# Performance work log

Hardware: AMD Instinct MI355X
Metric: run time of the kernel (lower is better)

## Reference

```python
import jax, jax.numpy as jnp
import numpy as np


def setup_inputs() -> dict:
    key = jax.random.key(0)
    N, E, LENGTH, DIM = 50000, 800000, 128, 128
    k1, k2, k3 = jax.random.split(key, 3)
    x = jax.random.normal(k1, (N, LENGTH), dtype=jnp.float32)
    edge_index = jax.random.randint(k2, (2, E), 0, N, dtype=jnp.int32)
    W = jax.random.normal(k3, (LENGTH, DIM), dtype=jnp.float32) / np.sqrt(LENGTH).astype(np.float32)
    b = jnp.zeros((DIM,), dtype=jnp.float32)
    return {"x": x, "edge_index": edge_index, "W": W, "b": b, "length": LENGTH, "dim": DIM}


def reference(x, edge_index, W, b, length, dim):
    # GCNConv(length, dim) with default add_self_loops + symmetric normalization,
    # then ReLU and softmax over the feature axis (dim=1).
    N = x.shape[0]
    src, dst = edge_index[0], edge_index[1]  # messages flow src -> dst (PyG source_to_target)
    loop = jnp.arange(N, dtype=src.dtype)
    src = jnp.concatenate([src, loop])
    dst = jnp.concatenate([dst, loop])
    # degree (incl. self-loops) computed on destination nodes, as in PyG gcn_norm
    deg = jax.ops.segment_sum(jnp.ones(dst.shape, dtype=x.dtype), dst, num_segments=N)
    dinv = jnp.where(deg > 0, jax.lax.rsqrt(deg), 0.0)
    norm = dinv[src] * dinv[dst]  # [E+N]
    xw = x @ W  # [N, dim] -- transform before propagate (in >= out here)
    msgs = xw[src] * norm[:, None]  # [E+N, dim] gather + scale
    out = jax.ops.segment_sum(msgs, dst, num_segments=N) + b  # scatter-add
    out = jax.nn.relu(out)
    return jax.nn.softmax(out, axis=1)
```

## Files before the change

kernel.cpp:

```cpp
#include <hip/hip_runtime.h>
#include <hip/hip_bf16.h>


#define KDIM 128
#define CAP 48
#define BSTRIDE 5120
#define GPAD 32

typedef __attribute__((ext_vector_type(8))) short bf16x8;
typedef __attribute__((ext_vector_type(4))) float f32x4;

__device__ __forceinline__ unsigned short f2bf(float f) {
    union { float f; unsigned u; } v; v.f = f;
    unsigned r = v.u + 0x7fff + ((v.u >> 16) & 1);
    return (unsigned short)(r >> 16);
}
__device__ __forceinline__ float bflo(unsigned u) {
    union { unsigned u; float f; } v; v.u = u << 16; return v.f;
}
__device__ __forceinline__ float bfhi(unsigned u) {
    union { unsigned u; float f; } v; v.u = u & 0xffff0000u; return v.f;
}

#define WPAD 72

__global__ __launch_bounds__(256) void fused_k(const float* __restrict__ x,
                                               const float* __restrict__ W,
                                               const int* __restrict__ src,
                                               const int* __restrict__ dst,
                                               int* __restrict__ gcount,
                                               unsigned int* __restrict__ gbuck,
                                               unsigned short* __restrict__ xwh,
                                               int N, int E, int GB, int nbuck) {
    __shared__ unsigned short Wl[128 * WPAD];
    __shared__ int hist[256];
    __shared__ int gbase_s[256];

    const int tid = threadIdx.x;

    if ((int)blockIdx.x >= GB) {
        int base = ((int)blockIdx.x - GB) * 2048;
        hist[tid] = 0;
        __syncthreads();

        unsigned ev[8];
        int bn[8], lr[8];
#pragma unroll
        for (int j = 0; j < 8; ++j) {
            int e = base + j * 256 + tid;
            bn[j] = -1;
            if (e < E) {
                int d = dst[e];
                int s = src[e];
                ev[j] = ((unsigned)d << 16) | (unsigned)s;
                bn[j] = d >> 8;
                lr[j] = atomicAdd(&hist[bn[j]], 1);
            }
        }
        __syncthreads();

        if (tid < nbuck && hist[tid] > 0)
            gbase_s[tid] = atomicAdd(&gcount[tid * GPAD], hist[tid]);
        __syncthreads();

#pragma unroll
        for (int j = 0; j < 8; ++j) {
            if (bn[j] >= 0) {
                int slot = gbase_s[bn[j]] + lr[j];
                if (slot < BSTRIDE)
                    gbuck[(size_t)bn[j] * BSTRIDE + slot] = ev[j];
            }
        }
        return;
    }

    const int lane = tid & 63;
    const int wv = tid >> 6;
    const int m15 = lane & 15;
    const int quad = lane >> 4;
    const int rbase = (int)blockIdx.x * 128;

    f32x4 acc[2][8];
#pragma unroll
    for (int st = 0; st < 2; ++st)
#pragma unroll
        for (int nb = 0; nb < 8; ++nb) acc[st][nb] = (f32x4){0.f, 0.f, 0.f, 0.f};

    for (int kc = 0; kc < KDIM; kc += 64) {
#pragma unroll
        for (int i = 0; i < 8; ++i) {
            int p = tid + 256 * i;
            int kk = p >> 5;
            int c4 = p & 31;
            float4 v = *(const float4*)(&W[(size_t)(kc + kk) * KDIM + c4 * 4]);
            int n0 = c4 * 4;
            Wl[(n0 + 0) * WPAD + kk] = f2bf(v.x);
            Wl[(n0 + 1) * WPAD + kk] = f2bf(v.y);
            Wl[(n0 + 2) * WPAD + kk] = f2bf(v.z);
            Wl[(n0 + 3) * WPAD + kk] = f2bf(v.w);
        }
        __syncthreads();

#pragma unroll
        for (int s2 = 0; s2 < 2; ++s2) {
            int k0 = kc + s2 * 32 + quad * 8;
            bf16x8 afr[2];
#pragma unroll
            for (int st = 0; st < 2; ++st) {
                int gr = rbase + wv * 32 + st * 16 + m15;
                int cr = min(gr, N - 1);
                const float4* xp = (const float4*)(&x[(size_t)cr * KDIM + k0]);
                float4 xa = xp[0], xb = xp[1];
                bf16x8 f;
                f[0] = (short)f2bf(xa.x); f[1] = (short)f2bf(xa.y);
                f[2] = (short)f2bf(xa.z); f[3] = (short)f2bf(xa.w);
                f[4] = (short)f2bf(xb.x); f[5] = (short)f2bf(xb.y);
                f[6] = (short)f2bf(xb.z); f[7] = (short)f2bf(xb.w);
                afr[st] = f;
            }
            int kk0 = s2 * 32 + quad * 8;
#pragma unroll
            for (int nb = 0; nb < 8; ++nb) {
                bf16x8 bfr = *(const bf16x8*)(&Wl[(nb * 16 + m15) * WPAD + kk0]);
#pragma unroll
                for (int st = 0; st < 2; ++st)
                    acc[st][nb] = __builtin_amdgcn_mfma_f32_16x16x32_bf16(
                        afr[st], bfr, acc[st][nb], 0, 0, 0);
            }
        }
        __syncthreads();
    }

#pragma unroll
    for (int st = 0; st < 2; ++st) {
        int rowbase = rbase + wv * 32 + st * 16 + quad * 4;
#pragma unroll
        for (int r = 0; r < 4; ++r) {
            int gr = rowbase + r;
            if (gr < N) {
#pragma unroll
                for (int nb = 0; nb < 8; ++nb)
                    xwh[(size_t)gr * KDIM + nb * 16 + m15] = f2bf(acc[st][nb][r]);
            }
        }
    }
}

__global__ __launch_bounds__(256) void build_k(const unsigned int* __restrict__ gbuck,
                                               const int* __restrict__ gcount,
                                               int* __restrict__ degi,
                                               unsigned short* __restrict__ csr,
                                               int N) {
    __shared__ unsigned int eb[BSTRIDE];
    __shared__ unsigned short cl[256 * CAP];
    __shared__ int cnts[256];

    const int tid = threadIdx.x;
    const int b = (int)blockIdx.x;
    const int cnt = min(gcount[b * GPAD], BSTRIDE);

    cnts[tid] = 0;
    for (int i = tid; i < cnt; i += 256) eb[i] = gbuck[(size_t)b * BSTRIDE + i];
    __syncthreads();

    for (int i = tid; i < cnt; i += 256) {
        unsigned e = eb[i];
        int j = (int)(e >> 16) & 255;
        int p = atomicAdd(&cnts[j], 1);
        if (p < CAP) cl[j * CAP + p] = (unsigned short)(e & 0xffffu);
    }
    __syncthreads();

    int d = b * 256 + tid;
    if (d < N) degi[d] = cnts[tid];

    int R = min(256, N - b * 256);
    const unsigned int* clu = (const unsigned int*)cl;
    unsigned int* csru = (unsigned int*)(csr + (size_t)b * 256 * CAP);
    int tot = R * (CAP / 2);
    for (int i = tid; i < tot; i += 256) csru[i] = clu[i];
}

__global__ __launch_bounds__(256) void gather_k(const unsigned short* __restrict__ xwh,
                                                const unsigned short* __restrict__ csr,
                                                const int* __restrict__ degi,
                                                const float* __restrict__ b,
                                                float* __restrict__ out, int N) {
    int node = (blockIdx.x * blockDim.x + threadIdx.x) >> 6;
    if (node >= N) return;
    int lane = threadIdx.x & 63;
    int h = lane >> 4;
    int c = lane & 15;

    int cnt = degi[node];
    int ccnt = min(cnt, CAP);
    float dn = rsqrtf((float)(cnt + 1));

    float a[8];
#pragma unroll
    for (int i = 0; i < 8; ++i) a[i] = 0.f;

    if (h == 0) {
        float sn = dn * dn;
        uint4 u = *(const uint4*)(&xwh[(size_t)node * KDIM + c * 8]);
        float4 b0 = *(const float4*)(&b[c * 8]);
        float4 b1 = *(const float4*)(&b[c * 8 + 4]);
        a[0] = bflo(u.x) * sn + b0.x; a[1] = bfhi(u.x) * sn + b0.y;
        a[2] = bflo(u.y) * sn + b0.z; a[3] = bfhi(u.y) * sn + b0.w;
        a[4] = bflo(u.z) * sn + b1.x; a[5] = bfhi(u.z) * sn + b1.y;
        a[6] = bflo(u.w) * sn + b1.z; a[7] = bfhi(u.w) * sn + b1.w;
    }

    int s_l = 0;
    float w_l = 0.f;
    if (lane < ccnt) {
        s_l = csr[(size_t)node * CAP + lane];
        w_l = rsqrtf((float)(degi[s_l] + 1));
    }

    int kmax = (ccnt + 3) >> 2;
#pragma unroll 4
    for (int k = 0; k < kmax; ++k) {
        int idx = 4 * k + h;
        int s = __shfl(s_l, idx);
        float nv = __shfl(w_l, idx) * dn;
        uint4 u = *(const uint4*)(&xwh[(size_t)s * KDIM + c * 8]);
        a[0] += bflo(u.x) * nv; a[1] += bfhi(u.x) * nv;
        a[2] += bflo(u.y) * nv; a[3] += bfhi(u.y) * nv;
        a[4] += bflo(u.z) * nv; a[5] += bfhi(u.z) * nv;
        a[6] += bflo(u.w) * nv; a[7] += bfhi(u.w) * nv;
    }

#pragma unroll
    for (int off = 16; off <= 32; off <<= 1) {
#pragma unroll
        for (int i = 0; i < 8; ++i) a[i] += __shfl_xor(a[i], off);
    }

    float mx = -1e30f;
#pragma unroll
    for (int i = 0; i < 8; ++i) {
        a[i] = fmaxf(a[i], 0.f);
        mx = fmaxf(mx, a[i]);
    }
#pragma unroll
    for (int off = 1; off < 16; off <<= 1) mx = fmaxf(mx, __shfl_xor(mx, off));
    float e[8], s = 0.f;
#pragma unroll
    for (int i = 0; i < 8; ++i) {
        e[i] = __expf(a[i] - mx);
        s += e[i];
    }
#pragma unroll
    for (int off = 1; off < 16; off <<= 1) s += __shfl_xor(s, off);
    float rs = 1.0f / s;
    if (h == 0) {
        float4 o0 = make_float4(e[0] * rs, e[1] * rs, e[2] * rs, e[3] * rs);
        float4 o1 = make_float4(e[4] * rs, e[5] * rs, e[6] * rs, e[7] * rs);
        *(float4*)(&out[(size_t)node * KDIM + c * 8]) = o0;
        *(float4*)(&out[(size_t)node * KDIM + c * 8 + 4]) = o1;
    }
}

extern "C" void kernel_launch(void* const* d_in, const int* in_sizes, int n_in,
                              void* d_out, int out_size, void* d_ws, size_t ws_size,
                              hipStream_t stream) {
    const float* x  = (const float*)d_in[0];
    const int*   ei = (const int*)d_in[1];
    const float* W  = (const float*)d_in[2];
    const float* b  = (const float*)d_in[3];

    const int N = in_sizes[0] / KDIM;
    const int E = in_sizes[1] / 2;
    const int* src = ei;
    const int* dst = ei + E;

    const int nbuck = (N + 255) >> 8;

    unsigned short* xwh    = (unsigned short*)d_ws;
    int*            degi   = (int*)(xwh + (size_t)N * KDIM);
    unsigned short* csr    = (unsigned short*)(degi + N);
    int*            gcount = (int*)(csr + (size_t)N * CAP);
    unsigned int*   gbuck  = (unsigned int*)(gcount + (size_t)nbuck * GPAD);
    float*          out    = (float*)d_out;

    hipMemsetAsync(gcount, 0, (size_t)nbuck * GPAD * sizeof(int), stream);

    const int GB = (N + 127) / 128;
    const int FB = (E + 2047) / 2048;
    fused_k<<<GB + FB, 256, 0, stream>>>(x, W, src, dst, gcount, gbuck, xwh, N, E, GB, nbuck);

    build_k<<<nbuck, 256, 0, stream>>>(gbuck, gcount, degi, csr, N);

    gather_k<<<(N + 3) / 4, 256, 0, stream>>>(xwh, csr, degi, b, out, N);
}
```

Measured before the change: 146.0 us.

## Replace global bucket atomics with per-block segmented buckets and precompute degree norms

Edge bucketing no longer uses global atomicAdd on per-bucket counters. Each edge block writes its edges into a private fixed-capacity segment per destination bucket, plus a count matrix, and the memset is removed. build_k then walks the segments per bucket, with one thread serially scanning each segment. It also stores rsqrt(deg+1) once so gather_k can load it instead of recomputing it. The trade-offs are a sparse, larger gbuck layout, uncoalesced serial segment reads in build_k, and a SEGCAP overflow risk.

```diff
diff --git a/kernel.cpp b/kernel.cpp
--- a/kernel.cpp
+++ b/kernel.cpp
@@ -4,8 +4,7 @@
 
 #define KDIM 128
 #define CAP 48
-#define BSTRIDE 5120
-#define GPAD 32
+#define SEGCAP 64
 
 typedef __attribute__((ext_vector_type(8))) short bf16x8;
 typedef __attribute__((ext_vector_type(4))) float f32x4;
@@ -28,18 +27,18 @@
                                                const float* __restrict__ W,
                                                const int* __restrict__ src,
                                                const int* __restrict__ dst,
-                                               int* __restrict__ gcount,
+                                               int* __restrict__ counts,
                                                unsigned int* __restrict__ gbuck,
                                                unsigned short* __restrict__ xwh,
-                                               int N, int E, int GB, int nbuck) {
+                                               int N, int E, int GB, int NG, int NB) {
     __shared__ unsigned short Wl[128 * WPAD];
     __shared__ int hist[256];
-    __shared__ int gbase_s[256];
 
     const int tid = threadIdx.x;
 
     if ((int)blockIdx.x >= GB) {
-        int base = ((int)blockIdx.x - GB) * 2048;
+        int g = (int)blockIdx.x - GB;
+        int base = g * 2048;
         hist[tid] = 0;
         __syncthreads();
 
@@ -59,18 +58,12 @@
         }
         __syncthreads();
 
-        if (tid < nbuck && hist[tid] > 0)
-            gbase_s[tid] = atomicAdd(&gcount[tid * GPAD], hist[tid]);
-        __syncthreads();
-
-#pragma unroll
-        for (int j = 0; j < 8; ++j) {
-            if (bn[j] >= 0) {
-                int slot = gbase_s[bn[j]] + lr[j];
-                if (slot < BSTRIDE)
-                    gbuck[(size_t)bn[j] * BSTRIDE + slot] = ev[j];
-            }
-        }
+        if (tid < NB) counts[tid * NG + g] = hist[tid];
+
+#pragma unroll
+        for (int j = 0; j < 8; ++j)
+            if (bn[j] >= 0 && lr[j] < SEGCAP)
+                gbuck[((size_t)bn[j] * NG + g) * SEGCAP + lr[j]] = ev[j];
         return;
     }
 
@@ -147,32 +140,38 @@
 }
 
 __global__ __launch_bounds__(256) void build_k(const unsigned int* __restrict__ gbuck,
-                                               const int* __restrict__ gcount,
+                                               const int* __restrict__ counts,
                                                int* __restrict__ degi,
+                                               float* __restrict__ dnv,
                                                unsigned short* __restrict__ csr,
-                                               int N) {
-    __shared__ unsigned int eb[BSTRIDE];
+                                               int N, int NG) {
     __shared__ unsigned short cl[256 * CAP];
     __shared__ int cnts[256];
 
     const int tid = threadIdx.x;
     const int b = (int)blockIdx.x;
-    const int cnt = min(gcount[b * GPAD], BSTRIDE);
 
     cnts[tid] = 0;
-    for (int i = tid; i < cnt; i += 256) eb[i] = gbuck[(size_t)b * BSTRIDE + i];
     __syncthreads();
 
-    for (int i = tid; i < cnt; i += 256) {
-        unsigned e = eb[i];
-        int j = (int)(e >> 16) & 255;
-        int p = atomicAdd(&cnts[j], 1);
-        if (p < CAP) cl[j * CAP + p] = (unsigned short)(e & 0xffffu);
+    for (int g = tid; g < NG; g += 256) {
+        int c = min(counts[b * NG + g], SEGCAP);
+        const unsigned int* seg = &gbuck[((size_t)b * NG + g) * SEGCAP];
+        for (int i = 0; i < c; ++i) {
+            unsigned e = seg[i];
+            int j = (int)(e >> 16) & 255;
+            int p = atomicAdd(&cnts[j], 1);
+            if (p < CAP) cl[j * CAP + p] = (unsigned short)(e & 0xffffu);
+        }
     }
     __syncthreads();
 
     int d = b * 256 + tid;
-    if (d < N) degi[d] = cnts[tid];
+    if (d < N) {
+        int c = cnts[tid];
+        degi[d] = c;
+        dnv[d] = rsqrtf((float)(c + 1));
+    }
 
     int R = min(256, N - b * 256);
     const unsigned int* clu = (const unsigned int*)cl;
@@ -184,6 +183,7 @@
 __global__ __launch_bounds__(256) void gather_k(const unsigned short* __restrict__ xwh,
                                                 const unsigned short* __restrict__ csr,
                                                 const int* __restrict__ degi,
+                                                const float* __restrict__ dnv,
                                                 const float* __restrict__ b,
                                                 float* __restrict__ out, int N) {
     int node = (blockIdx.x * blockDim.x + threadIdx.x) >> 6;
@@ -194,7 +194,7 @@
 
     int cnt = degi[node];
     int ccnt = min(cnt, CAP);
-    float dn = rsqrtf((float)(cnt + 1));
+    float dn = dnv[node];
 
     float a[8];
 #pragma unroll
@@ -215,7 +215,7 @@
     float w_l = 0.f;
     if (lane < ccnt) {
         s_l = csr[(size_t)node * CAP + lane];
-        w_l = rsqrtf((float)(degi[s_l] + 1));
+        w_l = dnv[s_l];
     }
 
     int kmax = (ccnt + 3) >> 2;
@@ -275,22 +275,21 @@
     const int* src = ei;
     const int* dst = ei + E;
 
-    const int nbuck = (N + 255) >> 8;
+    const int NB = (N + 255) >> 8;
+    const int NG = (E + 2047) / 2048;
 
     unsigned short* xwh    = (unsigned short*)d_ws;
     int*            degi   = (int*)(xwh + (size_t)N * KDIM);
-    unsigned short* csr    = (unsigned short*)(degi + N);
-    int*            gcount = (int*)(csr + (size_t)N * CAP);
-    unsigned int*   gbuck  = (unsigned int*)(gcount + (size_t)nbuck * GPAD);
+    float*          dnv    = (float*)(degi + N);
+    unsigned short* csr    = (unsigned short*)(dnv + N);
+    int*            counts = (int*)(csr + (size_t)N * CAP);
+    unsigned int*   gbuck  = (unsigned int*)(counts + (size_t)NB * NG);
     float*          out    = (float*)d_out;
 
-    hipMemsetAsync(gcount, 0, (size_t)nbuck * GPAD * sizeof(int), stream);
-
     const int GB = (N + 127) / 128;
-    const int FB = (E + 2047) / 2048;
-    fused_k<<<GB + FB, 256, 0, stream>>>(x, W, src, dst, gcount, gbuck, xwh, N, E, GB, nbuck);
-
-    build_k<<<nbuck, 256, 0, stream>>>(gbuck, gcount, degi, csr, N);
-
-    gather_k<<<(N + 3) / 4, 256, 0, stream>>>(xwh, csr, degi, b, out, N);
-}
+    fused_k<<<GB + NG, 256, 0, stream>>>(x, W, src, dst, counts, gbuck, xwh, N, E, GB, NG, NB);
+
+    build_k<<<NB, 256, 0, stream>>>(gbuck, counts, degi, dnv, csr, N, NG);
+
+    gather_k<<<(N + 3) / 4, 256, 0, stream>>>(xwh, csr, degi, dnv, b, out, N);
+}
```

Result: slower. 153.3 us (+5.0%).
